# Performance work log

Measured on AMD Instinct MI355X. Metric: run time of the kernel, lower is better.

## Reference

```python
import jax, jax.numpy as jnp
import numpy as np

N = 50000; E = 800000; G = 256
FIN = 64; EIN = 16; HC = 128; H = 2; C = 64; EF = 64; NB = 2
EPS = 1e-5
SQRT_C = np.float32(np.sqrt(C))


def elu(x):
    return jax.nn.elu(x)


def seg_softmax(logits, seg, num):
    # numerically stable softmax over groups defined by seg
    m = jax.ops.segment_max(logits, seg, num_segments=num)
    e = jnp.exp(logits - m[seg])
    s = jax.ops.segment_sum(e, seg, num_segments=num)
    return e / s[seg]


def graph_ln(x, batch, gamma, beta):
    # PyG LayerNorm(mode='graph'): stats over all nodes AND channels of each graph
    cnt = jax.ops.segment_sum(jnp.ones((x.shape[0],), x.dtype), batch, num_segments=G) * x.shape[1]
    cnt = jnp.maximum(cnt, 1.0)
    s = jax.ops.segment_sum(x.sum(-1), batch, num_segments=G)
    ss = jax.ops.segment_sum((x * x).sum(-1), batch, num_segments=G)
    mean = s / cnt
    var = jnp.maximum(ss / cnt - mean * mean, 0.0)
    xn = (x - mean[batch][:, None]) * jax.lax.rsqrt(var + EPS)[batch][:, None]
    return xn * gamma + beta


def tconv(x, ea, src, dst, wq, bq, wk, bk, wv, bv, we, wsk, bsk):
    # PyG TransformerConv (concat=True, beta=False, root_weight=True, dropout=0)
    q = (x @ wq + bq).reshape(N, H, C)
    k = (x @ wk + bk).reshape(N, H, C)
    v = (x @ wv + bv).reshape(N, H, C)
    e = (ea @ we).reshape(E, H, C)
    kj = k[src] + e
    alpha = jnp.einsum('ehc,ehc->eh', q[dst], kj) / SQRT_C
    alpha = seg_softmax(alpha, dst, N)  # scatter-softmax over destination nodes
    out = jax.ops.segment_sum((v[src] + e) * alpha[:, :, None], dst, num_segments=N)
    return out.reshape(N, HC) + x @ wsk + bsk


def setup_inputs():
    key = jax.random.key(0)
    ks = jax.random.split(key, 16)
    rn = lambda k, shape, sc: jax.random.normal(k, shape, jnp.float32) * sc
    s64 = 1.0 / np.sqrt(64.0); s128 = 1.0 / np.sqrt(128.0); s16 = 1.0 / np.sqrt(16.0)
    return {
        'x': rn(ks[0], (N, FIN), 1.0),
        'edge_attr': rn(ks[1], (E, EIN), 1.0),
        'edge_index': jax.random.randint(ks[2], (2, E), 0, N, jnp.int32),
        'batch': jnp.sort(jax.random.randint(ks[3], (N,), 0, G, jnp.int32)),
        'w0': rn(ks[4], (FIN, HC), s64), 'b0': jnp.zeros((HC,), jnp.float32),
        'we0': rn(ks[5], (EIN, EF), s16), 'be0': jnp.zeros((EF,), jnp.float32),
        'ln0_g': jnp.ones((HC,), jnp.float32), 'ln0_b': jnp.zeros((HC,), jnp.float32),
        'qkv_w': rn(ks[6], (NB, 2, 3, HC, HC), s128), 'qkv_b': jnp.zeros((NB, 2, 3, HC), jnp.float32),
        'edge_w': rn(ks[7], (NB, 2, EF, HC), s64),
        'skip_w': rn(ks[8], (NB, 2, HC, HC), s128), 'skip_b': jnp.zeros((NB, 2, HC), jnp.float32),
        'up_w': rn(ks[9], (NB, 2, EF, EF), s64), 'up_b': jnp.zeros((NB, 2, EF), jnp.float32),
        'ng': jnp.ones((NB, 2, HC), jnp.float32), 'nb': jnp.zeros((NB, 2, HC), jnp.float32),
        'sag_wrel': rn(ks[10], (NB, HC), s128), 'sag_brel': jnp.zeros((NB,), jnp.float32),
        'sag_wroot': rn(ks[11], (NB, HC), s128),
        're_w': rn(ks[12], (NB, EF, HC), s64), 're_b': jnp.zeros((NB, HC), jnp.float32),
    }


def reference(x, edge_attr, edge_index, batch, w0, b0, we0, be0, ln0_g, ln0_b,
              qkv_w, qkv_b, edge_w, skip_w, skip_b, up_w, up_b, ng, nb,
              sag_wrel, sag_brel, sag_wroot, re_w, re_b):
    src, dst = edge_index[0], edge_index[1]
    h = elu(graph_ln(x @ w0 + b0, batch, ln0_g, ln0_b))
    ea = elu(edge_attr @ we0 + be0)
    embs = []
    for i in range(NB):
        # ne_update: conv1 + graph-LN + lin_up on edges
        h = tconv(h, ea, src, dst,
                  qkv_w[i, 0, 0], qkv_b[i, 0, 0], qkv_w[i, 0, 1], qkv_b[i, 0, 1],
                  qkv_w[i, 0, 2], qkv_b[i, 0, 2], edge_w[i, 0], skip_w[i, 0], skip_b[i, 0])
        h = elu(graph_ln(h, batch, ng[i, 0], nb[i, 0]))
        ea = elu(ea @ up_w[i, 0] + up_b[i, 0])
        # conv2 + lin_up2
        h = tconv(h, ea, src, dst,
                  qkv_w[i, 1, 0], qkv_b[i, 1, 0], qkv_w[i, 1, 1], qkv_b[i, 1, 1],
                  qkv_w[i, 1, 2], qkv_b[i, 1, 2], edge_w[i, 1], skip_w[i, 1], skip_b[i, 1])
        ea2 = ea @ up_w[i, 1] + up_b[i, 1]
        # SAGPooling(min_score=-1) keeps all nodes: score = per-graph softmax of GraphConv
        aggr = jax.ops.segment_sum(h[src], dst, num_segments=N)
        sc = aggr @ sag_wrel[i] + sag_brel[i] + h @ sag_wroot[i]  # [N]
        sc = seg_softmax(sc, batch, G)
        emb = jax.ops.segment_sum(h * sc[:, None], batch, num_segments=G)
        emb_e = elu(jax.ops.segment_sum(ea2, batch[src], num_segments=G) @ re_w[i] + re_b[i])
        emb = emb * emb_e
        emb = elu(emb / jnp.maximum(jnp.linalg.norm(emb, axis=1, keepdims=True), 1e-12))
        embs.append(emb)
        h = elu(graph_ln(h, batch, ng[i, 1], nb[i, 1]))
        ea = elu(ea2)
    return 0.6 * embs[0] + 0.4 * embs[-1]
```

## Files before the change

kernel.cpp:

```cpp
#include <hip/hip_runtime.h>
#include <math.h>

#define NN 50000
#define EE 800000
#define GG 256

typedef unsigned short u16;
typedef unsigned int u32;
typedef __attribute__((ext_vector_type(4))) float f32x4;
typedef __attribute__((ext_vector_type(8))) short bf16x8;

__device__ __forceinline__ float elu_f(float x) { return x > 0.f ? x : expm1f(x); }

__device__ __forceinline__ unsigned fenc(float f) {
  unsigned b = __float_as_uint(f);
  return (b & 0x80000000u) ? ~b : (b | 0x80000000u);
}
__device__ __forceinline__ float fdec(unsigned u) {
  return __uint_as_float((u & 0x80000000u) ? (u ^ 0x80000000u) : ~u);
}
__device__ __forceinline__ u16 f2b(float f) {
  u32 u = __float_as_uint(f);
  u32 r = (u + 0x7fffu + ((u >> 16) & 1u)) >> 16;
  return (u16)r;
}
__device__ __forceinline__ float bf2f(u16 u) { return __uint_as_float(((u32)u) << 16); }
__device__ __forceinline__ float lo2f(u32 p) { return __uint_as_float(p << 16); }
__device__ __forceinline__ float hi2f(u32 p) { return __uint_as_float(p & 0xffff0000u); }

__device__ __forceinline__ float wred64(float v) {
#pragma unroll
  for (int m = 32; m; m >>= 1) v += __shfl_xor(v, m, 64);
  return v;
}

__global__ __launch_bounds__(256) void gemm_kernel(
    const float* __restrict__ A, const float* __restrict__ B,
    const float* __restrict__ bias, float* __restrict__ C,
    int M, int Nn, int K, int act, int accum) {
  __shared__ float As[16][68];
  __shared__ float Bs[16][68];
  const int bm = blockIdx.y * 64;
  const int bn = blockIdx.x * 64;
  const int tid = threadIdx.x;
  const int tx = tid & 15, ty = tid >> 4;
  const int lr = tid >> 2;
  const int lk = (tid & 3) << 2;
  float acc[4][4] = {};
  for (int k0 = 0; k0 < K; k0 += 16) {
    int arow = bm + lr;
    float4 a4 = {0.f, 0.f, 0.f, 0.f};
    if (arow < M) a4 = *reinterpret_cast<const float4*>(A + (size_t)arow * K + k0 + lk);
    As[lk + 0][lr] = a4.x; As[lk + 1][lr] = a4.y;
    As[lk + 2][lr] = a4.z; As[lk + 3][lr] = a4.w;
    float4 b4 = *reinterpret_cast<const float4*>(B + (size_t)(k0 + ty) * Nn + bn + tx * 4);
    *reinterpret_cast<float4*>(&Bs[ty][tx * 4]) = b4;
    __syncthreads();
#pragma unroll
    for (int kk = 0; kk < 16; ++kk) {
      float4 av = *reinterpret_cast<const float4*>(&As[kk][ty * 4]);
      float4 bv = *reinterpret_cast<const float4*>(&Bs[kk][tx * 4]);
      float a_[4] = {av.x, av.y, av.z, av.w};
      float b_[4] = {bv.x, bv.y, bv.z, bv.w};
#pragma unroll
      for (int ii = 0; ii < 4; ++ii)
#pragma unroll
        for (int jj = 0; jj < 4; ++jj)
          acc[ii][jj] = fmaf(a_[ii], b_[jj], acc[ii][jj]);
    }
    __syncthreads();
  }
#pragma unroll
  for (int ii = 0; ii < 4; ++ii) {
    int row = bm + ty * 4 + ii;
    if (row >= M) continue;
#pragma unroll
    for (int jj = 0; jj < 4; ++jj) {
      int col = bn + tx * 4 + jj;
      float val = acc[ii][jj];
      if (bias) val += bias[col];
      if (accum) val += C[(size_t)row * Nn + col];
      if (act) val = elu_f(val);
      C[(size_t)row * Nn + col] = val;
    }
  }
}

__global__ void csr_hist(const int* __restrict__ dst, int* __restrict__ deg) {
  int e = blockIdx.x * blockDim.x + threadIdx.x;
  if (e < EE) atomicAdd(&deg[dst[e]], 1);
}

__global__ void scan1(const int* __restrict__ deg, int* __restrict__ pre,
                      int* __restrict__ bsum, int n) {
  __shared__ int s[256];
  int t = threadIdx.x;
  int i = blockIdx.x * 256 + t;
  int v = (i < n) ? deg[i] : 0;
  s[t] = v;
  __syncthreads();
  for (int off = 1; off < 256; off <<= 1) {
    int tmp = (t >= off) ? s[t - off] : 0;
    __syncthreads();
    s[t] += tmp;
    __syncthreads();
  }
  if (i < n) pre[i] = s[t] - v;
  if (t == 255) bsum[blockIdx.x] = s[255];
}

__global__ void scan2(int* __restrict__ bsum, int nb) {
  __shared__ int s[256];
  int t = threadIdx.x;
  int v = (t < nb) ? bsum[t] : 0;
  s[t] = v;
  __syncthreads();
  for (int off = 1; off < 256; off <<= 1) {
    int tmp = (t >= off) ? s[t - off] : 0;
    __syncthreads();
    s[t] += tmp;
    __syncthreads();
  }
  if (t < nb) bsum[t] = s[t] - v;
}

__global__ void scan3(const int* __restrict__ pre, const int* __restrict__ bsum,
                      const int* __restrict__ deg, int* __restrict__ row_start,
                      int* __restrict__ cursor, int n) {
  int i = blockIdx.x * 256 + threadIdx.x;
  if (i < n) {
    int v = pre[i] + bsum[blockIdx.x];
    row_start[i] = v;
    cursor[i] = v;
    if (i == n - 1) row_start[n] = v + deg[i];
  }
}

__global__ void gstart_build(const int* __restrict__ batch, int* __restrict__ gstart) {
  int n = blockIdx.x * blockDim.x + threadIdx.x;
  if (n > NN) return;
  int b = (n < NN) ? batch[n] : GG;
  int pb = (n == 0) ? -1 : batch[n - 1];
  for (int g = pb + 1; g <= b; ++g) gstart[g] = n;
}

__global__ void csr_pos(const int* __restrict__ src, const int* __restrict__ dst,
                        int* __restrict__ cursor, int* __restrict__ csr_src,
                        int* __restrict__ epos) {
  int e = blockIdx.x * blockDim.x + threadIdx.x;
  if (e >= EE) return;
  int pos = atomicAdd(&cursor[dst[e]], 1);
  csr_src[pos] = src[e];
  epos[e] = pos;
}

__global__ void out_hist(const int* __restrict__ csr_src, int* __restrict__ odeg) {
  int pos = blockIdx.x * blockDim.x + threadIdx.x;
  if (pos < EE) atomicAdd(&odeg[csr_src[pos]], 1);
}

__global__ void out_fill(const int* __restrict__ csr_src, int* __restrict__ ocursor,
                         int* __restrict__ operm) {
  int pos = blockIdx.x * blockDim.x + threadIdx.x;
  if (pos < EE) {
    int slot = atomicAdd(&ocursor[csr_src[pos]], 1);
    operm[slot] = pos;
  }
}

__global__ void sgstart_build(const int* __restrict__ out_start, const int* __restrict__ gstart,
                              int* __restrict__ sg_start) {
  int t = blockIdx.x * blockDim.x + threadIdx.x;
  if (t <= GG) sg_start[t] = out_start[gstart[t]];
}

__global__ void build_we0frag(const float* __restrict__ we0, u16* __restrict__ wf_hi,
                              u16* __restrict__ wf_lo) {
  int idx = blockIdx.x * 256 + threadIdx.x;
  if (idx >= 2048) return;
  int j = idx & 7, lane = (idx >> 3) & 63, t = idx >> 9;
  int k = (lane >> 4) * 8 + j;
  int c = t * 16 + (lane & 15);
  float w = (k < 16) ? we0[(size_t)k * 64 + c] : 0.f;
  u16 hi = f2b(w);
  wf_hi[idx] = hi;
  wf_lo[idx] = f2b(w - bf2f(hi));
}

__global__ __launch_bounds__(256) void ea_enc_mfma(const float* __restrict__ edge_attr,
                                                   const u16* __restrict__ wf_hi,
                                                   const u16* __restrict__ wf_lo,
                                                   const float* __restrict__ be0,
                                                   const int* __restrict__ epos,
                                                   u16* __restrict__ ea) {
  int lane = threadIdx.x & 63;
  int gwave = (blockIdx.x * 256 + threadIdx.x) >> 6;
  int nwaves = (gridDim.x * 256) >> 6;
  bf16x8 bh[4], bl[4];
#pragma unroll
  for (int t = 0; t < 4; ++t) {
    bh[t] = *reinterpret_cast<const bf16x8*>(wf_hi + ((size_t)(t * 64 + lane)) * 8);
    bl[t] = *reinterpret_cast<const bf16x8*>(wf_lo + ((size_t)(t * 64 + lane)) * 8);
  }
  float bias_c[4];
#pragma unroll
  for (int t = 0; t < 4; ++t) bias_c[t] = be0[t * 16 + (lane & 15)];
  const int rif = lane & 15;
  const int kg = lane >> 4;
  for (int mt = gwave; mt < EE / 16; mt += nwaves) {
    int base = mt * 16;
    bf16x8 ah = {}, al = {};
    if (kg < 2) {
      const float* ap = edge_attr + (size_t)(base + rif) * 16 + kg * 8;
      float4 f0 = *reinterpret_cast<const float4*>(ap);
      float4 f1 = *reinterpret_cast<const float4*>(ap + 4);
      float fv[8] = {f0.x, f0.y, f0.z, f0.w, f1.x, f1.y, f1.z, f1.w};
#pragma unroll
      for (int jj = 0; jj < 8; ++jj) {
        u16 hi = f2b(fv[jj]);
        ah[jj] = (short)hi;
        al[jj] = (short)f2b(fv[jj] - bf2f(hi));
      }
    }
    f32x4 acc[4] = {};
#pragma unroll
    for (int t = 0; t < 4; ++t) {
      acc[t] = __builtin_amdgcn_mfma_f32_16x16x32_bf16(ah, bh[t], acc[t], 0, 0, 0);
      acc[t] = __builtin_amdgcn_mfma_f32_16x16x32_bf16(ah, bl[t], acc[t], 0, 0, 0);
      acc[t] = __builtin_amdgcn_mfma_f32_16x16x32_bf16(al, bh[t], acc[t], 0, 0, 0);
    }
#pragma unroll
    for (int rg = 0; rg < 4; ++rg) {
      int pr = epos[base + kg * 4 + rg];
#pragma unroll
      for (int t = 0; t < 4; ++t)
        ea[(size_t)pr * 64 + t * 16 + rif] = f2b(elu_f(acc[t][rg] + bias_c[t]));
    }
  }
}

__global__ __launch_bounds__(256) void ln_stats_block(const float* __restrict__ h,
                                                      const int* __restrict__ gstart,
                                                      float* __restrict__ gmean,
                                                      float* __restrict__ grstd) {
  __shared__ float ls[4], lss[4];
  int g = blockIdx.x, t = threadIdx.x;
  int n0 = gstart[g], n1 = gstart[g + 1];
  int total4 = (n1 - n0) * 32;
  const float4* base = (const float4*)(h + (size_t)n0 * 128);
  float s = 0.f, ss = 0.f;
  for (int i = t; i < total4; i += 256) {
    float4 v = base[i];
    s += v.x + v.y + v.z + v.w;
    ss += v.x * v.x + v.y * v.y + v.z * v.z + v.w * v.w;
  }
  s = wred64(s);
  ss = wred64(ss);
  if ((t & 63) == 0) { ls[t >> 6] = s; lss[t >> 6] = ss; }
  __syncthreads();
  if (t == 0) {
    float S = ls[0] + ls[1] + ls[2] + ls[3];
    float SS = lss[0] + lss[1] + lss[2] + lss[3];
    float cnt = fmaxf((float)(n1 - n0) * 128.f, 1.0f);
    float mean = S / cnt;
    float var = fmaxf(SS / cnt - mean * mean, 0.f);
    gmean[g] = mean;
    grstd[g] = rsqrtf(var + 1e-5f);
  }
}

__global__ __launch_bounds__(256) void ln_apply(const float* __restrict__ in,
                                                u16* __restrict__ out_hi,
                                                u16* __restrict__ out_lo,
                                                const int* __restrict__ batch,
                                                const float* __restrict__ gmean,
                                                const float* __restrict__ grstd,
                                                const float* __restrict__ gamma,
                                                const float* __restrict__ beta) {
  int idx = blockIdx.x * blockDim.x + threadIdx.x;
  if (idx >= NN * 32) return;
  int n = idx >> 5, c4 = (idx & 31) * 4;
  int g = batch[n];
  float mean = gmean[g], rstd = grstd[g];
  float4 xv = *reinterpret_cast<const float4*>(in + (size_t)n * 128 + c4);
  float4 gv = *reinterpret_cast<const float4*>(gamma + c4);
  float4 bv = *reinterpret_cast<const float4*>(beta + c4);
  float v0 = elu_f((xv.x - mean) * rstd * gv.x + bv.x);
  float v1 = elu_f((xv.y - mean) * rstd * gv.y + bv.y);
  float v2 = elu_f((xv.z - mean) * rstd * gv.z + bv.z);
  float v3 = elu_f((xv.w - mean) * rstd * gv.w + bv.w);
  u16 h0 = f2b(v0), h1 = f2b(v1), h2 = f2b(v2), h3 = f2b(v3);
  uint2 hi = {(u32)h0 | ((u32)h1 << 16), (u32)h2 | ((u32)h3 << 16)};
  uint2 lo = {(u32)f2b(v0 - bf2f(h0)) | ((u32)f2b(v1 - bf2f(h1)) << 16),
              (u32)f2b(v2 - bf2f(h2)) | ((u32)f2b(v3 - bf2f(h3)) << 16)};
  *reinterpret_cast<uint2*>(out_hi + (size_t)n * 128 + c4) = hi;
  *reinterpret_cast<uint2*>(out_lo + (size_t)n * 128 + c4) = lo;
}

__global__ void build_wqe(const float* __restrict__ wq, const float* __restrict__ bq,
                          const float* __restrict__ we, float* __restrict__ WQE,
                          float* __restrict__ bqe) {
  int col = threadIdx.x;
  int row = blockIdx.x;
  int hh = col >> 6, j = col & 63;
  const float* wrow = (row < 128) ? (wq + (size_t)row * 128) : bq;
  float acc = 0.f;
  for (int c = 0; c < 64; ++c) acc += wrow[hh * 64 + c] * we[(size_t)j * 128 + hh * 64 + c];
  if (row < 128) WQE[(size_t)row * 128 + col] = acc;
  else bqe[col] = acc;
}

__global__ void build_wfrag2(const float* __restrict__ wq, const float* __restrict__ wk,
                             const float* __restrict__ wv, const float* __restrict__ WQE,
                             const float* __restrict__ wsk, const float* __restrict__ we,
                             const float* __restrict__ bq, const float* __restrict__ bk,
                             const float* __restrict__ bv, const float* __restrict__ bqe,
                             const float* __restrict__ bsk,
                             u16* __restrict__ Wfrag_hi, u16* __restrict__ Wfrag_lo,
                             u16* __restrict__ wef_hi, u16* __restrict__ wef_lo,
                             float* __restrict__ ball) {
  int idx = blockIdx.x * 256 + threadIdx.x;
  if (idx < 81920) {
    int j = idx & 7, lane = (idx >> 3) & 63, rest = idx >> 9;
    int tg = rest % 40, s = rest / 40;
    int k = s * 32 + (lane >> 4) * 8 + j;
    int col = tg * 16 + (lane & 15);
    int sel = col >> 7, c = col & 127;
    const float* src = sel == 0 ? wq : sel == 1 ? wk : sel == 2 ? wv : sel == 3 ? WQE : wsk;
    float w = src[(size_t)k * 128 + c];
    u16 hi = f2b(w);
    Wfrag_hi[idx] = hi;
    Wfrag_lo[idx] = f2b(w - bf2f(hi));
  } else if (idx < 90112) {
    int i2 = idx - 81920;
    int j = i2 & 7, lane = (i2 >> 3) & 63, rest = i2 >> 9;
    int t = rest & 3, hh = (rest >> 2) & 1, s = rest >> 3;
    int k = s * 32 + (lane >> 4) * 8 + j;
    int col = hh * 64 + t * 16 + (lane & 15);
    float w = we[(size_t)k * 128 + col];
    u16 hi = f2b(w);
    wef_hi[i2] = hi;
    wef_lo[i2] = f2b(w - bf2f(hi));
  }
  if (idx < 640) {
    int sel = idx >> 7, c = idx & 127;
    const float* s2 = sel == 0 ? bq : sel == 1 ? bk : sel == 2 ? bv : sel == 3 ? bqe : bsk;
    ball[idx] = s2[c];
  }
}

__global__ void build_upfrag(const float* __restrict__ up, u16* __restrict__ upfrag) {
  int idx = blockIdx.x * 256 + threadIdx.x;
  if (idx >= 4096) return;
  int j = idx & 7, lane = (idx >> 3) & 63, st = idx >> 9;
  int s = st >> 2, t = st & 3;
  int k = s * 32 + (lane >> 4) * 8 + j;
  int c = t * 16 + (lane & 15);
  upfrag[idx] = f2b(up[k * 64 + c]);
}

__global__ void build_w2(const float* __restrict__ up, const float* __restrict__ ub,
                         const float* __restrict__ re_w, float* __restrict__ W2,
                         float* __restrict__ bvec, float* __restrict__ gsum_in) {
  int idx = blockIdx.x * 256 + threadIdx.x;
  if (idx < 64 * 128) {
    int k_ = idx >> 7, c = idx & 127;
    float a = 0.f;
    for (int j = 0; j < 64; ++j) a = fmaf(up[k_ * 64 + j], re_w[j * 128 + c], a);
    W2[idx] = a;
  } else if (idx < 64 * 128 + 128) {
    int c = idx - 64 * 128;
    float a = 0.f;
    for (int j = 0; j < 64; ++j) a = fmaf(ub[j], re_w[j * 128 + c], a);
    bvec[c] = a;
  }
  if (idx < GG * 64) gsum_in[idx] = 0.f;
}

__global__ __launch_bounds__(256) void node_gemm(const u16* __restrict__ h_hi,
                                                 const u16* __restrict__ h_lo,
                                                 const u16* __restrict__ Wfrag_hi,
                                                 const u16* __restrict__ Wfrag_lo,
                                                 const float* __restrict__ ball,
                                                 u16* __restrict__ nodebuf,
                                                 float* __restrict__ hn) {
  int tid = threadIdx.x;
  int lane = tid & 63;
  int wv = tid >> 6;
  int cb = blockIdx.x;
  int rbase = blockIdx.y * 64 + wv * 16;
  int rif = lane & 15, kg = lane >> 4;
  f32x4 acc[4] = {};
  int arow = rbase + rif;
  bool rowok = arow < NN;
  const u16* aph = h_hi + (size_t)arow * 128 + kg * 8;
  const u16* apl = h_lo + (size_t)arow * 128 + kg * 8;
#pragma unroll
  for (int s = 0; s < 4; ++s) {
    bf16x8 ah = {}, al = {};
    if (rowok) {
      ah = *reinterpret_cast<const bf16x8*>(aph + s * 32);
      al = *reinterpret_cast<const bf16x8*>(apl + s * 32);
    }
#pragma unroll
    for (int t = 0; t < 4; ++t) {
      size_t fo = ((size_t)((s * 40 + cb * 4 + t) * 64 + lane)) * 8;
      bf16x8 bh = *reinterpret_cast<const bf16x8*>(Wfrag_hi + fo);
      bf16x8 bl = *reinterpret_cast<const bf16x8*>(Wfrag_lo + fo);
      acc[t] = __builtin_amdgcn_mfma_f32_16x16x32_bf16(ah, bh, acc[t], 0, 0, 0);
      acc[t] = __builtin_amdgcn_mfma_f32_16x16x32_bf16(ah, bl, acc[t], 0, 0, 0);
      acc[t] = __builtin_amdgcn_mfma_f32_16x16x32_bf16(al, bh, acc[t], 0, 0, 0);
    }
  }
#pragma unroll
  for (int t = 0; t < 4; ++t) {
    int col = (cb * 4 + t) * 16 + rif;
    float bia = ball[col];
#pragma unroll
    for (int rg = 0; rg < 4; ++rg) {
      int row = rbase + kg * 4 + rg;
      if (row < NN) {
        float val = acc[t][rg] + bia;
        if (col < 512) {
          int idx;
          if (col < 128) idx = col;
          else if (col < 256) { int c1 = col - 128; idx = 256 + ((c1 >> 1) << 2) + (c1 & 1); }
          else if (col < 384) { int c2 = col - 256; idx = 256 + ((c2 >> 1) << 2) + 2 + (c2 & 1); }
          else idx = 128 + (col - 384);
          nodebuf[(size_t)row * 512 + idx] = f2b(val);
        } else {
          hn[(size_t)row * 128 + col - 512] = val;
        }
      }
    }
  }
}

__global__ __launch_bounds__(256) void edge_gemm(u16* __restrict__ ea,
                                                 const u16* __restrict__ upfrag,
                                                 const float* __restrict__ ub) {
  int lane = threadIdx.x & 63;
  int gwave = (blockIdx.x * 256 + threadIdx.x) >> 6;
  int nwaves = (gridDim.x * 256) >> 6;
  bf16x8 bfrag[2][4];
#pragma unroll
  for (int s = 0; s < 2; ++s)
#pragma unroll
    for (int t = 0; t < 4; ++t)
      bfrag[s][t] = *reinterpret_cast<const bf16x8*>(upfrag + ((size_t)((s * 4 + t) * 64 + lane)) * 8);
  float bias_c[4];
#pragma unroll
  for (int t = 0; t < 4; ++t) bias_c[t] = ub[t * 16 + (lane & 15)];
  const int rif = lane & 15;
  const int kg = lane >> 4;
  for (int mt = gwave; mt < EE / 16; mt += nwaves) {
    size_t rowbase = (size_t)mt * 16;
    const u16* arow = ea + (rowbase + rif) * 64;
    bf16x8 a0 = *reinterpret_cast<const bf16x8*>(arow + kg * 8);
    bf16x8 a1 = *reinterpret_cast<const bf16x8*>(arow + 32 + kg * 8);
    f32x4 acc[4] = {};
#pragma unroll
    for (int t = 0; t < 4; ++t) {
      acc[t] = __builtin_amdgcn_mfma_f32_16x16x32_bf16(a0, bfrag[0][t], acc[t], 0, 0, 0);
      acc[t] = __builtin_amdgcn_mfma_f32_16x16x32_bf16(a1, bfrag[1][t], acc[t], 0, 0, 0);
    }
#pragma unroll
    for (int t = 0; t < 4; ++t)
#pragma unroll
      for (int rg = 0; rg < 4; ++rg) {
        float val = acc[t][rg] + bias_c[t];
        ea[(rowbase + kg * 4 + rg) * 64 + t * 16 + rif] = f2b(elu_f(val));
      }
  }
}

__global__ __launch_bounds__(256) void bd_gemm(const u16* __restrict__ r_hi,
                                               const u16* __restrict__ r_lo,
                                               const u16* __restrict__ wef_hi,
                                               const u16* __restrict__ wef_lo,
                                               float* __restrict__ hn) {
  int tid = threadIdx.x;
  int lane = tid & 63;
  int w = blockIdx.x * 4 + (tid >> 6);
  if (w >= NN / 16) return;
  int rif = lane & 15, kg = lane >> 4;
  size_t rowbase = (size_t)w * 16;
  const u16* ahb = r_hi + (rowbase + rif) * 128;
  const u16* alb = r_lo + (rowbase + rif) * 128;
  f32x4 acc[2][4] = {};
#pragma unroll
  for (int hh = 0; hh < 2; ++hh)
#pragma unroll
    for (int s = 0; s < 2; ++s) {
      int ko = hh * 64 + s * 32 + kg * 8;
      bf16x8 ah = *reinterpret_cast<const bf16x8*>(ahb + ko);
      bf16x8 al = *reinterpret_cast<const bf16x8*>(alb + ko);
#pragma unroll
      for (int t = 0; t < 4; ++t) {
        size_t fo = ((size_t)((((s * 2 + hh) * 4 + t)) * 64 + lane)) * 8;
        bf16x8 bh = *reinterpret_cast<const bf16x8*>(wef_hi + fo);
        bf16x8 bl = *reinterpret_cast<const bf16x8*>(wef_lo + fo);
        acc[hh][t] = __builtin_amdgcn_mfma_f32_16x16x32_bf16(ah, bh, acc[hh][t], 0, 0, 0);
        acc[hh][t] = __builtin_amdgcn_mfma_f32_16x16x32_bf16(ah, bl, acc[hh][t], 0, 0, 0);
        acc[hh][t] = __builtin_amdgcn_mfma_f32_16x16x32_bf16(al, bh, acc[hh][t], 0, 0, 0);
      }
    }
#pragma unroll
  for (int hh = 0; hh < 2; ++hh)
#pragma unroll
    for (int t = 0; t < 4; ++t)
#pragma unroll
      for (int rg = 0; rg < 4; ++rg) {
        size_t row = rowbase + kg * 4 + rg;
        int col = hh * 64 + t * 16 + rif;
        hn[row * 128 + col] += acc[hh][t][rg];
      }
}

__global__ __launch_bounds__(256) void gsum_pre(const u16* __restrict__ ea,
                                                const int* __restrict__ sg_start,
                                                const int* __restrict__ sg_perm,
                                                float* __restrict__ gsum_in) {
  __shared__ float red[8][64];
  int g = blockIdx.x, t = threadIdx.x;
  int c2 = t & 31;
  int rgrp = t >> 5;
  int gr = blockIdx.y * 8 + rgrp;
  int p0 = sg_start[g], p1 = sg_start[g + 1];
  float slo = 0.f, shi = 0.f;
  for (int i = p0 + gr; i < p1; i += 128) {
    int pos = sg_perm[i];
    u32 w = ((const u32*)ea)[(size_t)pos * 32 + c2];
    slo += lo2f(w);
    shi += hi2f(w);
  }
  red[rgrp][c2 * 2] = slo;
  red[rgrp][c2 * 2 + 1] = shi;
  __syncthreads();
  if (t < 64) {
    float a = 0.f;
#pragma unroll
    for (int rr = 0; rr < 8; ++rr) a += red[rr][t];
    atomicAdd(&gsum_in[(size_t)g * 64 + t], a);
  }
}

__global__ void emb_e_kernel(const float* __restrict__ gsum_in, const int* __restrict__ sg_start,
                             const float* __restrict__ W2, const float* __restrict__ bvec,
                             const float* __restrict__ re_b, float* __restrict__ embE) {
  int g = blockIdx.x, c = threadIdx.x;
  float cnt = (float)(sg_start[g + 1] - sg_start[g]);
  float a = re_b[c] + cnt * bvec[c];
  for (int k_ = 0; k_ < 64; ++k_) a = fmaf(gsum_in[(size_t)g * 64 + k_], W2[k_ * 128 + c], a);
  embE[(size_t)g * 128 + c] = elu_f(a);
}

__global__ __launch_bounds__(256) void attn_node(const u32* __restrict__ nb32,
                                                 const u32* __restrict__ ea32,
                                                 const int* __restrict__ row_start,
                                                 const int* __restrict__ csr_src,
                                                 float* __restrict__ hn,
                                                 u32* __restrict__ r_hi,
                                                 u32* __restrict__ r_lo) {
  int d = (blockIdx.x * blockDim.x + threadIdx.x) >> 6;
  if (d >= NN) return;
  int lane = threadIdx.x & 63;
  int grp = lane >> 4;
  int li = lane & 15;
  int qi = li * 4;
  int eai = (li & 7) * 4;
  int ridx = ((li >> 3) << 5) + ((li & 7) << 2);
  int p0 = row_start[d], p1 = row_start[d + 1];
  if (p0 == p1) {
    if (grp == 0) {
      uint4 z = {0u, 0u, 0u, 0u};
      *reinterpret_cast<uint4*>(r_hi + (size_t)d * 64 + ridx) = z;
      *reinterpret_cast<uint4*>(r_lo + (size_t)d * 64 + ridx) = z;
    }
    return;
  }
  size_t dbase = (size_t)d * 256;
  uint4 qp = *reinterpret_cast<const uint4*>(nb32 + dbase + qi);
  uint4 qep = *reinterpret_cast<const uint4*>(nb32 + dbase + 64 + qi);
  float q_[8] = {lo2f(qp.x), hi2f(qp.x), lo2f(qp.y), hi2f(qp.y),
                 lo2f(qp.z), hi2f(qp.z), lo2f(qp.w), hi2f(qp.w)};
  float g_[8] = {lo2f(qep.x), hi2f(qep.x), lo2f(qep.y), hi2f(qep.y),
                 lo2f(qep.z), hi2f(qep.z), lo2f(qep.w), hi2f(qep.w)};
  int cnt = p1 - p0;
  float m = -3.4e38f, ss = 0.f;
  float a_[8] = {}, r_[8] = {};
  int i = grp;
  bool vld = i < cnt;
  int pc = vld ? p0 + i : p0;
  int sc = csr_src[pc];
  const u32* kp = nb32 + (size_t)sc * 256 + 128 + qi * 2;
  uint4 kva = *reinterpret_cast<const uint4*>(kp);
  uint4 kvb = *reinterpret_cast<const uint4*>(kp + 4);
  uint4 ev = *reinterpret_cast<const uint4*>(ea32 + (size_t)pc * 32 + eai);
  int nIter = (cnt + 3) >> 2;
  for (int j = 0; j < nIter; ++j) {
    int i2 = i + 4;
    bool nvld = i2 < cnt;
    int pn = nvld ? p0 + i2 : p0;
    int sn = csr_src[pn];
    const u32* kpn = nb32 + (size_t)sn * 256 + 128 + qi * 2;
    uint4 kvan = *reinterpret_cast<const uint4*>(kpn);
    uint4 kvbn = *reinterpret_cast<const uint4*>(kpn + 4);
    uint4 evn = *reinterpret_cast<const uint4*>(ea32 + (size_t)pn * 32 + eai);
    float e_[8] = {lo2f(ev.x), hi2f(ev.x), lo2f(ev.y), hi2f(ev.y),
                   lo2f(ev.z), hi2f(ev.z), lo2f(ev.w), hi2f(ev.w)};
    float kk[8] = {lo2f(kva.x), hi2f(kva.x), lo2f(kva.z), hi2f(kva.z),
                   lo2f(kvb.x), hi2f(kvb.x), lo2f(kvb.z), hi2f(kvb.z)};
    float vv[8] = {lo2f(kva.y), hi2f(kva.y), lo2f(kva.w), hi2f(kva.w),
                   lo2f(kvb.y), hi2f(kvb.y), lo2f(kvb.w), hi2f(kvb.w)};
    float p = 0.f;
#pragma unroll
    for (int t = 0; t < 8; ++t) p = fmaf(q_[t], kk[t], fmaf(g_[t], e_[t], p));
#pragma unroll
    for (int mm = 1; mm <= 4; mm <<= 1) p += __shfl_xor(p, mm, 64);
    float lg = vld ? p * 0.125f : -3.4e38f;
    float mn = fmaxf(m, lg);
    float f = __expf(m - mn), w = __expf(lg - mn);
    ss = ss * f + w;
#pragma unroll
    for (int t = 0; t < 8; ++t) {
      a_[t] = fmaf(w, vv[t], a_[t] * f);
      r_[t] = fmaf(w, e_[t], r_[t] * f);
    }
    m = mn;
    i = i2; vld = nvld; kva = kvan; kvb = kvbn; ev = evn;
  }
#pragma unroll
  for (int mk = 16; mk <= 32; mk <<= 1) {
    float mo = __shfl_xor(m, mk, 64);
    float so = __shfl_xor(ss, mk, 64);
    float ao[8], ro[8];
#pragma unroll
    for (int t = 0; t < 8; ++t) {
      ao[t] = __shfl_xor(a_[t], mk, 64);
      ro[t] = __shfl_xor(r_[t], mk, 64);
    }
    float mn = fmaxf(m, mo);
    float fs = __expf(m - mn), fo = __expf(mo - mn);
    ss = ss * fs + so * fo;
#pragma unroll
    for (int t = 0; t < 8; ++t) {
      a_[t] = a_[t] * fs + ao[t] * fo;
      r_[t] = r_[t] * fs + ro[t] * fo;
    }
    m = mn;
  }
  if (grp == 0) {
    float inv = 1.f / ss;
    float* hp = hn + (size_t)d * 128 + li * 8;
    float4 h0 = *reinterpret_cast<float4*>(hp);
    float4 h1 = *reinterpret_cast<float4*>(hp + 4);
    h0.x += a_[0] * inv; h0.y += a_[1] * inv; h0.z += a_[2] * inv; h0.w += a_[3] * inv;
    h1.x += a_[4] * inv; h1.y += a_[5] * inv; h1.z += a_[6] * inv; h1.w += a_[7] * inv;
    *reinterpret_cast<float4*>(hp) = h0;
    *reinterpret_cast<float4*>(hp + 4) = h1;
    float rv[8];
    u16 rh16[8];
#pragma unroll
    for (int t = 0; t < 8; ++t) { rv[t] = r_[t] * inv; rh16[t] = f2b(rv[t]); }
    uint4 rh = {(u32)rh16[0] | ((u32)rh16[1] << 16), (u32)rh16[2] | ((u32)rh16[3] << 16),
                (u32)rh16[4] | ((u32)rh16[5] << 16), (u32)rh16[6] | ((u32)rh16[7] << 16)};
    uint4 rl;
    u32 rl16[8];
#pragma unroll
    for (int t = 0; t < 8; ++t) rl16[t] = (u32)f2b(rv[t] - bf2f(rh16[t]));
    rl.x = rl16[0] | (rl16[1] << 16); rl.y = rl16[2] | (rl16[3] << 16);
    rl.z = rl16[4] | (rl16[5] << 16); rl.w = rl16[6] | (rl16[7] << 16);
    *reinterpret_cast<uint4*>(r_hi + (size_t)d * 64 + ridx) = rh;
    *reinterpret_cast<uint4*>(r_lo + (size_t)d * 64 + ridx) = rl;
  }
}

__global__ __launch_bounds__(256) void node_dots(const float* __restrict__ hn,
                                                 const float* __restrict__ wrel,
                                                 const float* __restrict__ wroot,
                                                 float* __restrict__ hrel,
                                                 float* __restrict__ troot,
                                                 unsigned* __restrict__ gm,
                                                 float* __restrict__ gs) {
  int tid0 = blockIdx.x * blockDim.x + threadIdx.x;
  if (tid0 < GG) gm[tid0] = 0u;
  else if (tid0 < 2 * GG) gs[tid0 - GG] = 0.f;
  int n = tid0 >> 6;
  if (n >= NN) return;
  int lane = threadIdx.x & 63;
  float x0 = hn[(size_t)n * 128 + lane], x1 = hn[(size_t)n * 128 + 64 + lane];
  float tr = wred64(x0 * wrel[lane] + x1 * wrel[64 + lane]);
  float tt = wred64(x0 * wroot[lane] + x1 * wroot[64 + lane]);
  if (lane == 0) { hrel[n] = tr; troot[n] = tt; }
}

__global__ __launch_bounds__(256) void sag_gather(const float* __restrict__ hrel,
                                                  const float* __restrict__ troot,
                                                  const float* __restrict__ brel,
                                                  const int* __restrict__ row_start,
                                                  const int* __restrict__ csr_src,
                                                  const int* __restrict__ batch,
                                                  float* __restrict__ sc, unsigned* __restrict__ gm) {
  int n = blockIdx.x * blockDim.x + threadIdx.x;
  if (n >= NN) return;
  float s = 0.f;
  int p1 = row_start[n + 1];
  for (int pos = row_start[n]; pos < p1; ++pos) s += hrel[csr_src[pos]];
  float v = s + troot[n] + brel[0];
  sc[n] = v;
  atomicMax(&gm[batch[n]], fenc(v));
}

__global__ __launch_bounds__(256) void sag_exp(const float* __restrict__ sc,
                                               const int* __restrict__ batch,
                                               const unsigned* __restrict__ gm,
                                               float* __restrict__ gs, float* __restrict__ scp) {
  int n = blockIdx.x * blockDim.x + threadIdx.x;
  if (n >= NN) return;
  int g = batch[n];
  float p = __expf(sc[n] - fdec(gm[g]));
  scp[n] = p;
  atomicAdd(&gs[g], p);
}

__global__ void emb_block(const float* __restrict__ hn, const float* __restrict__ scp,
                          const float* __restrict__ gs, const int* __restrict__ gstart,
                          const float* __restrict__ embE, float* __restrict__ dstv) {
  __shared__ float part[2];
  int g = blockIdx.x, c = threadIdx.x;
  int n0 = gstart[g], n1 = gstart[g + 1];
  float invg = 1.f / gs[g];
  float acc = 0.f;
  for (int n = n0; n < n1; ++n) acc = fmaf(hn[(size_t)n * 128 + c], scp[n] * invg, acc);
  float val = acc * embE[(size_t)g * 128 + c];
  float sq = val * val;
#pragma unroll
  for (int mm = 32; mm; mm >>= 1) sq += __shfl_xor(sq, mm, 64);
  if ((c & 63) == 0) part[c >> 6] = sq;
  __syncthreads();
  float nrm = sqrtf(part[0] + part[1]);
  dstv[(size_t)g * 128 + c] = elu_f(val / fmaxf(nrm, 1e-12f));
}

__global__ void final_combine(const float* __restrict__ e0, const float* __restrict__ e1,
                              float* __restrict__ out) {
  int idx = blockIdx.x * blockDim.x + threadIdx.x;
  if (idx >= GG * 128) return;
  out[idx] = 0.6f * e0[idx] + 0.4f * e1[idx];
}

extern "C" void kernel_launch(void* const* d_in, const int* in_sizes, int n_in,
                              void* d_out, int out_size, void* d_ws, size_t ws_size,
                              hipStream_t stream) {
  const float* x = (const float*)d_in[0];
  const float* edge_attr = (const float*)d_in[1];
  const int* edge_index = (const int*)d_in[2];
  const int* batch = (const int*)d_in[3];
  const float* w0 = (const float*)d_in[4];
  const float* b0 = (const float*)d_in[5];
  const float* we0 = (const float*)d_in[6];
  const float* be0 = (const float*)d_in[7];
  const float* ln0_g = (const float*)d_in[8];
  const float* ln0_b = (const float*)d_in[9];
  const float* qkv_w = (const float*)d_in[10];
  const float* qkv_b = (const float*)d_in[11];
  const float* edge_w = (const float*)d_in[12];
  const float* skip_w = (const float*)d_in[13];
  const float* skip_b = (const float*)d_in[14];
  const float* up_w = (const float*)d_in[15];
  const float* up_b = (const float*)d_in[16];
  const float* ng = (const float*)d_in[17];
  const float* nbeta = (const float*)d_in[18];
  const float* sag_wrel = (const float*)d_in[19];
  const float* sag_brel = (const float*)d_in[20];
  const float* sag_wroot = (const float*)d_in[21];
  const float* re_w = (const float*)d_in[22];
  const float* re_b = (const float*)d_in[23];
  const int* srcp = edge_index;
  const int* dstp = edge_index + EE;
  float* out = (float*)d_out;
  (void)in_sizes; (void)n_in;

  float* ws = (float*)d_ws;
  size_t o = 0;
  auto alloc = [&](size_t n) { n = (n + 3) & ~(size_t)3; float* p = ws + o; o += n; return p; };
  u16* h_hi = (u16*)alloc((size_t)NN * 64);
  u16* h_lo = (u16*)alloc((size_t)NN * 64);
  float* hn = alloc((size_t)NN * 128);
  u32* r_hi = (u32*)alloc((size_t)NN * 64);
  u32* r_lo = (u32*)alloc((size_t)NN * 64);
  u16* nodebuf = (u16*)alloc((size_t)NN * 256);
  u16* ea = (u16*)alloc((size_t)EE * 32);
  int* csr_src = (int*)alloc(EE);
  int* epos = (int*)alloc(EE);
  int* deg = (int*)alloc(NN);
  int* pre = (int*)alloc(NN);
  int* bsum = (int*)alloc(256);
  int* row_start = (int*)alloc(NN + 1);
  int* cursor = (int*)alloc(NN);
  int* out_start = (int*)alloc(NN + 1);
  int* gstart = (int*)alloc(GG + 1);
  int* sg_perm = (int*)alloc(EE);
  int* sg_start = (int*)alloc(GG + 1);
  float* gsum_in = alloc(GG * 64);
  float* W2 = alloc(64 * 128);
  float* bvec = alloc(128);
  u16* upfrag = (u16*)alloc(2048);
  u16* Wfrag_hi = (u16*)alloc(40960);
  u16* Wfrag_lo = (u16*)alloc(40960);
  u16* wef_hi = (u16*)alloc(4096);
  u16* wef_lo = (u16*)alloc(4096);
  u16* wef0_hi = (u16*)alloc(1024);
  u16* wef0_lo = (u16*)alloc(1024);
  unsigned* gm = (unsigned*)alloc(GG);
  float* gs = alloc(GG);
  float* gmean = alloc(GG);
  float* grstd = alloc(GG);
  float* WQE = alloc(128 * 128);
  float* bqe = alloc(128);
  float* ball = alloc(640);
  float* hrel = alloc(NN);
  float* troot = alloc(NN);
  float* sc = alloc(NN);
  float* scp = alloc(NN);
  float* embE = alloc(GG * 128);
  float* embs0 = alloc(GG * 128);
  float* embs1 = alloc(GG * 128);

  const size_t need = o * sizeof(float);
  if (ws_size < need) {
    hipMemsetAsync(d_out, 0, (size_t)out_size * sizeof(float), stream);
    return;
  }
  const int NSCAN = (NN + 255) / 256;

  auto gemm = [&](const float* A, const float* B, const float* bias, float* C,
                  int M, int Nn, int K, int act, int accum) {
    dim3 g((Nn + 63) / 64, (M + 63) / 64);
    gemm_kernel<<<g, 256, 0, stream>>>(A, B, bias, C, M, Nn, K, act, accum);
  };
  auto ex_scan = [&](const int* degp, int* startp, int* curp) {
    scan1<<<NSCAN, 256, 0, stream>>>(degp, pre, bsum, NN);
    scan2<<<1, 256, 0, stream>>>(bsum, NSCAN);
    scan3<<<NSCAN, 256, 0, stream>>>(pre, bsum, degp, startp, curp, NN);
  };
  auto graph_ln = [&](const float* in, const float* gamma, const float* beta) {
    ln_stats_block<<<GG, 256, 0, stream>>>(in, gstart, gmean, grstd);
    ln_apply<<<NN * 32 / 256, 256, 0, stream>>>(in, h_hi, h_lo, batch, gmean, grstd, gamma, beta);
  };
  auto tconv = [&](int il) {
    const float* wq = qkv_w + (size_t)(il * 3 + 0) * 128 * 128;
    const float* wk = qkv_w + (size_t)(il * 3 + 1) * 128 * 128;
    const float* wv = qkv_w + (size_t)(il * 3 + 2) * 128 * 128;
    const float* bq = qkv_b + (il * 3 + 0) * 128;
    const float* bk = qkv_b + (il * 3 + 1) * 128;
    const float* bv = qkv_b + (il * 3 + 2) * 128;
    const float* we = edge_w + (size_t)il * 64 * 128;
    const float* wsk = skip_w + (size_t)il * 128 * 128;
    const float* bsk = skip_b + il * 128;
    build_wqe<<<129, 128, 0, stream>>>(wq, bq, we, WQE, bqe);
    build_wfrag2<<<352, 256, 0, stream>>>(wq, wk, wv, WQE, wsk, we, bq, bk, bv, bqe, bsk,
                                          Wfrag_hi, Wfrag_lo, wef_hi, wef_lo, ball);
    dim3 ng2(10, (NN + 63) / 64);
    node_gemm<<<ng2, 256, 0, stream>>>(h_hi, h_lo, Wfrag_hi, Wfrag_lo, ball, nodebuf, hn);
    attn_node<<<NN / 4, 256, 0, stream>>>((const u32*)nodebuf, (const u32*)ea, row_start,
                                          csr_src, hn, r_hi, r_lo);
    bd_gemm<<<(NN / 16 + 3) / 4, 256, 0, stream>>>((const u16*)r_hi, (const u16*)r_lo,
                                                   wef_hi, wef_lo, hn);
  };
  auto ea_mlp = [&](int il) {
    build_upfrag<<<16, 256, 0, stream>>>(up_w + (size_t)il * 4096, upfrag);
    edge_gemm<<<2048, 256, 0, stream>>>(ea, upfrag, up_b + il * 64);
  };

  hipMemsetAsync(deg, 0, NN * sizeof(int), stream);
  csr_hist<<<(EE + 255) / 256, 256, 0, stream>>>(dstp, deg);
  ex_scan(deg, row_start, cursor);
  gstart_build<<<(NN + 256) / 256, 256, 0, stream>>>(batch, gstart);
  csr_pos<<<(EE + 255) / 256, 256, 0, stream>>>(srcp, dstp, cursor, csr_src, epos);
  build_we0frag<<<8, 256, 0, stream>>>(we0, wef0_hi, wef0_lo);
  ea_enc_mfma<<<2048, 256, 0, stream>>>(edge_attr, wef0_hi, wef0_lo, be0, epos, ea);
  hipMemsetAsync(deg, 0, NN * sizeof(int), stream);
  out_hist<<<(EE + 255) / 256, 256, 0, stream>>>(csr_src, deg);
  ex_scan(deg, out_start, cursor);
  out_fill<<<(EE + 255) / 256, 256, 0, stream>>>(csr_src, cursor, sg_perm);
  sgstart_build<<<2, 256, 0, stream>>>(out_start, gstart, sg_start);
  gemm(x, w0, b0, hn, NN, 128, 64, 0, 0);
  graph_ln(hn, ln0_g, ln0_b);

  for (int i = 0; i < 2; ++i) {
    tconv(i * 2 + 0);
    graph_ln(hn, ng + (i * 2) * 128, nbeta + (i * 2) * 128);
    ea_mlp(i * 2);
    tconv(i * 2 + 1);
    build_w2<<<64, 256, 0, stream>>>(up_w + (size_t)(i * 2 + 1) * 4096,
                                     up_b + (i * 2 + 1) * 64,
                                     re_w + (size_t)i * 64 * 128, W2, bvec, gsum_in);
    dim3 gsg(GG, 16);
    gsum_pre<<<gsg, 256, 0, stream>>>(ea, sg_start, sg_perm, gsum_in);
    if (i == 0) ea_mlp(i * 2 + 1);
    node_dots<<<NN / 4, 256, 0, stream>>>(hn, sag_wrel + i * 128, sag_wroot + i * 128,
                                          hrel, troot, gm, gs);
    sag_gather<<<(NN + 255) / 256, 256, 0, stream>>>(hrel, troot, sag_brel + i, row_start,
                                                     csr_src, batch, sc, gm);
    sag_exp<<<(NN + 255) / 256, 256, 0, stream>>>(sc, batch, gm, gs, scp);
    emb_e_kernel<<<GG, 128, 0, stream>>>(gsum_in, sg_start, W2, bvec, re_b + i * 128, embE);
    emb_block<<<GG, 128, 0, stream>>>(hn, scp, gs, gstart, embE, i == 0 ? embs0 : embs1);
    if (i == 0) graph_ln(hn, ng + (i * 2 + 1) * 128, nbeta + (i * 2 + 1) * 128);
  }
  final_combine<<<GG * 128 / 256, 256, 0, stream>>>(embs0, embs1, out);
}
```

Measured before the change: 1.752 ms.

## Reuse node GEMM A fragments across all column blocks and split K/V layout

The node GEMM now launches one block per 64-row tile and loops over all 10 column blocks, loading the h_hi/h_lo A fragments once and reusing them instead of reloading them in 10 separate blocks. The nodebuf layout for K and V changes from interleaved pairs to two contiguous 128-column halves. The attention kernel reads keys and values as two contiguous 16-byte loads at offsets qi and qi+64, with simpler unpacking. This cuts redundant A-matrix reads. In exchange the grid has ten times fewer blocks and each wave runs a longer serial loop, which may lower parallelism.

```diff
diff --git a/kernel.cpp b/kernel.cpp
--- a/kernel.cpp
+++ b/kernel.cpp
@@ -387,49 +387,51 @@
   int tid = threadIdx.x;
   int lane = tid & 63;
   int wv = tid >> 6;
-  int cb = blockIdx.x;
-  int rbase = blockIdx.y * 64 + wv * 16;
+  int rbase = blockIdx.x * 64 + wv * 16;
   int rif = lane & 15, kg = lane >> 4;
-  f32x4 acc[4] = {};
   int arow = rbase + rif;
   bool rowok = arow < NN;
   const u16* aph = h_hi + (size_t)arow * 128 + kg * 8;
   const u16* apl = h_lo + (size_t)arow * 128 + kg * 8;
+  bf16x8 ah[4], al[4];
 #pragma unroll
   for (int s = 0; s < 4; ++s) {
-    bf16x8 ah = {}, al = {};
+    ah[s] = bf16x8{};
+    al[s] = bf16x8{};
     if (rowok) {
-      ah = *reinterpret_cast<const bf16x8*>(aph + s * 32);
-      al = *reinterpret_cast<const bf16x8*>(apl + s * 32);
+      ah[s] = *reinterpret_cast<const bf16x8*>(aph + s * 32);
+      al[s] = *reinterpret_cast<const bf16x8*>(apl + s * 32);
+    }
+  }
+  for (int cb = 0; cb < 10; ++cb) {
+    f32x4 acc[4] = {};
+#pragma unroll
+    for (int s = 0; s < 4; ++s) {
+#pragma unroll
+      for (int t = 0; t < 4; ++t) {
+        size_t fo = ((size_t)((s * 40 + cb * 4 + t) * 64 + lane)) * 8;
+        bf16x8 bh = *reinterpret_cast<const bf16x8*>(Wfrag_hi + fo);
+        bf16x8 bl = *reinterpret_cast<const bf16x8*>(Wfrag_lo + fo);
+        acc[t] = __builtin_amdgcn_mfma_f32_16x16x32_bf16(ah[s], bh, acc[t], 0, 0, 0);
+        acc[t] = __builtin_amdgcn_mfma_f32_16x16x32_bf16(ah[s], bl, acc[t], 0, 0, 0);
+        acc[t] = __builtin_amdgcn_mfma_f32_16x16x32_bf16(al[s], bh, acc[t], 0, 0, 0);
+      }
     }
 #pragma unroll
     for (int t = 0; t < 4; ++t) {
-      size_t fo = ((size_t)((s * 40 + cb * 4 + t) * 64 + lane)) * 8;
-      bf16x8 bh = *reinterpret_cast<const bf16x8*>(Wfrag_hi + fo);
-      bf16x8 bl = *reinterpret_cast<const bf16x8*>(Wfrag_lo + fo);
-      acc[t] = __builtin_amdgcn_mfma_f32_16x16x32_bf16(ah, bh, acc[t], 0, 0, 0);
-      acc[t] = __builtin_amdgcn_mfma_f32_16x16x32_bf16(ah, bl, acc[t], 0, 0, 0);
-      acc[t] = __builtin_amdgcn_mfma_f32_16x16x32_bf16(al, bh, acc[t], 0, 0, 0);
-    }
-  }
-#pragma unroll
-  for (int t = 0; t < 4; ++t) {
-    int col = (cb * 4 + t) * 16 + rif;
-    float bia = ball[col];
-#pragma unroll
-    for (int rg = 0; rg < 4; ++rg) {
-      int row = rbase + kg * 4 + rg;
-      if (row < NN) {
-        float val = acc[t][rg] + bia;
-        if (col < 512) {
-          int idx;
-          if (col < 128) idx = col;
-          else if (col < 256) { int c1 = col - 128; idx = 256 + ((c1 >> 1) << 2) + (c1 & 1); }
-          else if (col < 384) { int c2 = col - 256; idx = 256 + ((c2 >> 1) << 2) + 2 + (c2 & 1); }
-          else idx = 128 + (col - 384);
-          nodebuf[(size_t)row * 512 + idx] = f2b(val);
-        } else {
-          hn[(size_t)row * 128 + col - 512] = val;
+      int col = (cb * 4 + t) * 16 + rif;
+      float bia = ball[col];
+#pragma unroll
+      for (int rg = 0; rg < 4; ++rg) {
+        int row = rbase + kg * 4 + rg;
+        if (row < NN) {
+          float val = acc[t][rg] + bia;
+          if (col < 512) {
+            int idx = (col < 128) ? col : (col < 384 ? col + 128 : col - 256);
+            nodebuf[(size_t)row * 512 + idx] = f2b(val);
+          } else {
+            hn[(size_t)row * 128 + col - 512] = val;
+          }
         }
       }
     }
@@ -593,9 +595,9 @@
   bool vld = i < cnt;
   int pc = vld ? p0 + i : p0;
   int sc = csr_src[pc];
-  const u32* kp = nb32 + (size_t)sc * 256 + 128 + qi * 2;
-  uint4 kva = *reinterpret_cast<const uint4*>(kp);
-  uint4 kvb = *reinterpret_cast<const uint4*>(kp + 4);
+  const u32* kp = nb32 + (size_t)sc * 256 + 128 + qi;
+  uint4 kvk = *reinterpret_cast<const uint4*>(kp);
+  uint4 kvv = *reinterpret_cast<const uint4*>(kp + 64);
   uint4 ev = *reinterpret_cast<const uint4*>(ea32 + (size_t)pc * 32 + eai);
   int nIter = (cnt + 3) >> 2;
   for (int j = 0; j < nIter; ++j) {
@@ -603,16 +605,16 @@
     bool nvld = i2 < cnt;
     int pn = nvld ? p0 + i2 : p0;
     int sn = csr_src[pn];
-    const u32* kpn = nb32 + (size_t)sn * 256 + 128 + qi * 2;
-    uint4 kvan = *reinterpret_cast<const uint4*>(kpn);
-    uint4 kvbn = *reinterpret_cast<const uint4*>(kpn + 4);
+    const u32* kpn = nb32 + (size_t)sn * 256 + 128 + qi;
+    uint4 kvkn = *reinterpret_cast<const uint4*>(kpn);
+    uint4 kvvn = *reinterpret_cast<const uint4*>(kpn + 64);
     uint4 evn = *reinterpret_cast<const uint4*>(ea32 + (size_t)pn * 32 + eai);
     float e_[8] = {lo2f(ev.x), hi2f(ev.x), lo2f(ev.y), hi2f(ev.y),
                    lo2f(ev.z), hi2f(ev.z), lo2f(ev.w), hi2f(ev.w)};
-    float kk[8] = {lo2f(kva.x), hi2f(kva.x), lo2f(kva.z), hi2f(kva.z),
-                   lo2f(kvb.x), hi2f(kvb.x), lo2f(kvb.z), hi2f(kvb.z)};
-    float vv[8] = {lo2f(kva.y), hi2f(kva.y), lo2f(kva.w), hi2f(kva.w),
-                   lo2f(kvb.y), hi2f(kvb.y), lo2f(kvb.w), hi2f(kvb.w)};
+    float kk[8] = {lo2f(kvk.x), hi2f(kvk.x), lo2f(kvk.y), hi2f(kvk.y),
+                   lo2f(kvk.z), hi2f(kvk.z), lo2f(kvk.w), hi2f(kvk.w)};
+    float vv[8] = {lo2f(kvv.x), hi2f(kvv.x), lo2f(kvv.y), hi2f(kvv.y),
+                   lo2f(kvv.z), hi2f(kvv.z), lo2f(kvv.w), hi2f(kvv.w)};
     float p = 0.f;
 #pragma unroll
     for (int t = 0; t < 8; ++t) p = fmaf(q_[t], kk[t], fmaf(g_[t], e_[t], p));
@@ -628,7 +630,7 @@
       r_[t] = fmaf(w, e_[t], r_[t] * f);
     }
     m = mn;
-    i = i2; vld = nvld; kva = kvan; kvb = kvbn; ev = evn;
+    i = i2; vld = nvld; kvk = kvkn; kvv = kvvn; ev = evn;
   }
 #pragma unroll
   for (int mk = 16; mk <= 32; mk <<= 1) {
@@ -862,8 +864,8 @@
     build_wqe<<<129, 128, 0, stream>>>(wq, bq, we, WQE, bqe);
     build_wfrag2<<<352, 256, 0, stream>>>(wq, wk, wv, WQE, wsk, we, bq, bk, bv, bqe, bsk,
                                           Wfrag_hi, Wfrag_lo, wef_hi, wef_lo, ball);
-    dim3 ng2(10, (NN + 63) / 64);
-    node_gemm<<<ng2, 256, 0, stream>>>(h_hi, h_lo, Wfrag_hi, Wfrag_lo, ball, nodebuf, hn);
+    node_gemm<<<(NN + 63) / 64, 256, 0, stream>>>(h_hi, h_lo, Wfrag_hi, Wfrag_lo, ball,
+                                                  nodebuf, hn);
     attn_node<<<NN / 4, 256, 0, stream>>>((const u32*)nodebuf, (const u32*)ea, row_start,
                                           csr_src, hn, r_hi, r_lo);
     bd_gemm<<<(NN / 16 + 3) / 4, 256, 0, stream>>>((const u16*)r_hi, (const u16*)r_lo,
```

New measurement: 1.695 ms. 1.03x faster.
